# Optimization experiments

Hardware: AMD Instinct MI355X
Metric: run time of the kernel (lower is better)

The kernel has to match this reference:

```python
import jax, jax.numpy as jnp
import numpy as np
import math

N_HEAD = 8
LN_EPS = 1e-5


def _layernorm(x, g, b):
    mu = jnp.mean(x, axis=-1, keepdims=True)
    var = jnp.mean(jnp.square(x - mu), axis=-1, keepdims=True)
    return (x - mu) / jnp.sqrt(var + LN_EPS) * g + b


def setup_inputs() -> dict:
    key0 = jax.random.key(0)
    ks = jax.random.split(key0, 12)
    B, L, D, E = 4, 512, 256, 5  # batch, agents, n_embd, edge_feats_dim

    def w(k, shape):
        return jax.random.normal(k, shape, dtype=jnp.float32) * 0.02

    return {
        "key": jax.random.normal(ks[0], (B, L, D), jnp.float32),
        "value": jax.random.normal(ks[1], (B, L, D), jnp.float32),
        "query": jax.random.normal(ks[2], (B, L, D), jnp.float32),
        "atten_masks": jax.random.randint(ks[3], (B, L, L), 0, 2).astype(jnp.int32),
        "edge_feats": jax.random.normal(ks[4], (B, L, L, E), jnp.float32),
        # Linear weights stored [in, out] so forward is x @ W + b
        "Wk": w(ks[5], (D, D)), "bk": jnp.zeros((D,), jnp.float32),
        "Wq": w(ks[6], (D, D)), "bq": jnp.zeros((D,), jnp.float32),
        "Wv": w(ks[7], (D, D)), "bv": jnp.zeros((D,), jnp.float32),
        "Wp": w(ks[8], (D, D)), "bp": jnp.zeros((D,), jnp.float32),
        "We1": w(ks[9], (E, D)), "be1": jnp.zeros((D,), jnp.float32),
        "ln_g": jnp.ones((D,), jnp.float32), "ln_b": jnp.zeros((D,), jnp.float32),
        "We2": w(ks[10], (D, N_HEAD)), "be2": jnp.zeros((N_HEAD,), jnp.float32),
    }


def reference(key, value, query, atten_masks, edge_feats,
              Wk, bk, Wq, bq, Wv, bv, Wp, bp,
              We1, be1, ln_g, ln_b, We2, be2):
    B, L, D = query.shape
    hd = D // N_HEAD
    # QKV projections -> [B, H, L, hd]
    q = (query @ Wq + bq).reshape(B, L, N_HEAD, hd).transpose(0, 2, 1, 3)
    k = (key @ Wk + bk).reshape(B, L, N_HEAD, hd).transpose(0, 2, 1, 3)
    v = (value @ Wv + bv).reshape(B, L, N_HEAD, hd).transpose(0, 2, 1, 3)
    # scaled attention scores [B, H, L, L]
    att = jnp.einsum('bhqd,bhkd->bhqk', q, k) * (1.0 / math.sqrt(hd))
    # edge-feature additive bias: Linear -> ReLU -> LayerNorm -> Linear(per-head)
    e = jax.nn.relu(edge_feats @ We1 + be1)          # [B, L, L, D]
    e = _layernorm(e, ln_g, ln_b)
    e = e @ We2 + be2                                # [B, L, L, H]
    att = att + e.transpose(0, 3, 1, 2)
    # additive mask (0 -> -inf), softmax over keys
    att = jnp.where(atten_masks[:, None, :, :] == 0, -jnp.inf, att)
    att = jax.nn.softmax(att, axis=-1)
    y = jnp.einsum('bhqk,bhkd->bhqd', att, v)        # [B, H, L, hd]
    y = y.transpose(0, 2, 1, 3).reshape(B, L, D)
    return y @ Wp + bp
```

## Files before the change

### kernel.cpp

```cpp
#include <hip/hip_runtime.h>
#include <hip/hip_bf16.h>

#define L_SEQ 512
#define D_EMB 256
#define NH 8
#define HD 32
#define LL (L_SEQ * L_SEQ)

typedef __attribute__((ext_vector_type(8))) short short8;
typedef __attribute__((ext_vector_type(4))) float f32x4;
typedef unsigned short ushort;

__device__ __forceinline__ float bf2f(ushort u) {
    unsigned int x = ((unsigned int)u) << 16;
    float f;
    __builtin_memcpy(&f, &x, 4);
    return f;
}
__device__ __forceinline__ ushort f2bf(float x) {
    __hip_bfloat16 h = __float2bfloat16(x);
    ushort u;
    __builtin_memcpy(&u, &h, 2);
    return u;
}
__device__ __forceinline__ unsigned int fbits(float x) {
    unsigned int u;
    __builtin_memcpy(&u, &x, 4);
    return u;
}
__device__ __forceinline__ float asf(unsigned int u) {
    float f;
    __builtin_memcpy(&f, &u, 4);
    return f;
}
__device__ __forceinline__ unsigned int pack_bf16rnd(float a, float b) {
    return __builtin_amdgcn_perm(fbits(b) + 0x8000u, fbits(a) + 0x8000u, 0x07060302u);
}
__device__ __forceinline__ uint2 cvt_hilo2(float v0, float v1) {
    unsigned int hi = pack_bf16rnd(v0, v1);
    float h0 = asf(hi << 16);
    float h1 = asf(hi & 0xffff0000u);
    unsigned int lo = pack_bf16rnd(v0 - h0, v1 - h1);
    uint2 r; r.x = hi; r.y = lo;
    return r;
}

__global__ __launch_bounds__(256) void prep_kernel(
    const float* __restrict__ We1, const float* __restrict__ be1,
    const float* __restrict__ g,   const float* __restrict__ bta,
    const float* __restrict__ We2, const float* __restrict__ be2,
    ushort* __restrict__ W1G, ushort* __restrict__ B2G, float* __restrict__ tail)
{
    int t = threadIdx.x;
    __shared__ float red[16][256];
    float gd = g[t], bd = bta[t];
#pragma unroll
    for (int h = 0; h < 8; ++h) {
        float w2 = We2[t * 8 + h];
        red[h][t] = gd * w2;
        red[8 + h][t] = bd * w2;
    }
    __syncthreads();
    for (int off = 128; off > 0; off >>= 1) {
        if (t < off) {
#pragma unroll
            for (int row = 0; row < 16; ++row) red[row][t] += red[row][t + off];
        }
        __syncthreads();
    }
    if (t < 8) {
        tail[t] = red[t][0];
        tail[8 + t] = red[8 + t][0] + be2[t];
    }
    if (t >= 16 && t < 32) tail[t] = 0.f;

    for (int idx = t; idx < 8192; idx += 256) {
        int j = idx & 7, lane = (idx >> 3) & 63, tile = idx >> 9;
        int m = lane & 15, q = lane >> 4;
        int k = q * 8 + j;
        int d = tile * 16 + m;
        float v = 0.f;
        bool lo = false;
        if (k < 5)        v = We1[k * 256 + d];
        else if (k < 10)  { v = We1[(k - 5) * 256 + d]; lo = true; }
        else if (k < 15)  v = We1[(k - 10) * 256 + d];
        else if (k == 15) v = be1[d];
        else if (k == 16) { v = be1[d]; lo = true; }
        ushort hi = f2bf(v);
        W1G[idx] = lo ? f2bf(v - bf2f(hi)) : hi;
    }
    for (int idx = t; idx < 4096; idx += 256) {
        int j = idx & 7, lane = (idx >> 3) & 63, kc = idx >> 9;
        int n = lane & 15, q = lane >> 4;
        int d = kc * 32 + q * 8 + j;
        ushort out;
        if (n < 8)       out = f2bf(g[d] * We2[d * 8 + n]);
        else if (n == 8) out = 0x3F80;
        else             out = 0;
        B2G[idx] = out;
    }
}

__global__ __launch_bounds__(256) void prep_w(
    const float* __restrict__ Wq, const float* __restrict__ Wk,
    const float* __restrict__ Wv, const float* __restrict__ Wp,
    ushort* __restrict__ WThi, ushort* __restrict__ WTlo)
{
    int w = blockIdx.x;
    const float* W = (w == 0) ? Wq : (w == 1) ? Wk : (w == 2) ? Wv : Wp;
    ushort* dh = WThi + (size_t)w * 65536;
    ushort* dl = WTlo + (size_t)w * 65536;

    int tid = threadIdx.x;
    int n = blockIdx.y * 16 + (tid >> 4);
    int k0 = (tid & 15) * 16;

    ushort hbuf[16], lbuf[16];
#pragma unroll
    for (int kk = 0; kk < 16; ++kk) {
        float v = W[(size_t)(k0 + kk) * 256 + n];
        unsigned int hb = fbits(v) + 0x8000u;
        ushort hi = (ushort)(hb >> 16);
        float res = v - bf2f(hi);
        hbuf[kk] = hi;
        lbuf[kk] = (ushort)((fbits(res) + 0x8000u) >> 16);
    }
    *(short8*)(dh + (size_t)n * 256 + k0)     = *(short8*)&hbuf[0];
    *(short8*)(dh + (size_t)n * 256 + k0 + 8) = *(short8*)&hbuf[8];
    *(short8*)(dl + (size_t)n * 256 + k0)     = *(short8*)&lbuf[0];
    *(short8*)(dl + (size_t)n * 256 + k0 + 8) = *(short8*)&lbuf[8];
}

__global__ __launch_bounds__(256) void gemm_mfma(
    const float* __restrict__ A0, const ushort* __restrict__ H0,
    const ushort* __restrict__ L0, const float* __restrict__ b0,
    float* __restrict__ C0,
    const float* __restrict__ A1, const ushort* __restrict__ H1,
    const ushort* __restrict__ L1, const float* __restrict__ b1,
    float* __restrict__ C1,
    const float* __restrict__ A2, const ushort* __restrict__ H2,
    const ushort* __restrict__ L2, const float* __restrict__ b2,
    float* __restrict__ C2)
{
    const float* A; const ushort* BH; const ushort* BL;
    const float* bias; float* C;
    if (blockIdx.z == 0)      { A = A0; BH = H0; BL = L0; bias = b0; C = C0; }
    else if (blockIdx.z == 1) { A = A1; BH = H1; BL = L1; bias = b1; C = C1; }
    else                      { A = A2; BH = H2; BL = L2; bias = b2; C = C2; }

    __shared__ ushort Ahi[64][40];
    __shared__ ushort Alo[64][40];

    int tid = threadIdx.x;
    int wv = tid >> 6, lane = tid & 63;
    int m = lane & 15, quad = lane >> 4;
    int bm = blockIdx.x * 64, bn = blockIdx.y * 64;

    int sm = tid >> 2, sg = (tid & 3) * 8;
    const float* Arow = A + (size_t)(bm + sm) * 256 + sg;

    int nrow = bn + wv * 16 + m;
    const ushort* bhp = BH + (size_t)nrow * 256 + quad * 8;
    const ushort* blp = BL + (size_t)nrow * 256 + quad * 8;

    f32x4 acc[4];
#pragma unroll
    for (int mt = 0; mt < 4; ++mt) acc[mt] = (f32x4){0.f, 0.f, 0.f, 0.f};

    for (int k0 = 0; k0 < 256; k0 += 32) {
        float4 a0 = *(const float4*)(Arow + k0);
        float4 a1 = *(const float4*)(Arow + k0 + 4);
        uint2 c0 = cvt_hilo2(a0.x, a0.y);
        uint2 c1 = cvt_hilo2(a0.z, a0.w);
        uint2 c2 = cvt_hilo2(a1.x, a1.y);
        uint2 c3 = cvt_hilo2(a1.z, a1.w);
        if (k0) __syncthreads();
        uint4 hq; hq.x = c0.x; hq.y = c1.x; hq.z = c2.x; hq.w = c3.x;
        uint4 lq; lq.x = c0.y; lq.y = c1.y; lq.z = c2.y; lq.w = c3.y;
        *(uint4*)&Ahi[sm][sg] = hq;
        *(uint4*)&Alo[sm][sg] = lq;
        __syncthreads();

        short8 bhi = *(const short8*)(bhp + k0);
        short8 blo = *(const short8*)(blp + k0);
#pragma unroll
        for (int mt = 0; mt < 4; ++mt) {
            short8 ahi = *(const short8*)&Ahi[mt * 16 + m][quad * 8];
            short8 alo = *(const short8*)&Alo[mt * 16 + m][quad * 8];
            acc[mt] = __builtin_amdgcn_mfma_f32_16x16x32_bf16(ahi, blo, acc[mt], 0, 0, 0);
            acc[mt] = __builtin_amdgcn_mfma_f32_16x16x32_bf16(alo, bhi, acc[mt], 0, 0, 0);
            acc[mt] = __builtin_amdgcn_mfma_f32_16x16x32_bf16(ahi, bhi, acc[mt], 0, 0, 0);
        }
    }

    float bn_bias = bias[nrow];
#pragma unroll
    for (int mt = 0; mt < 4; ++mt) {
#pragma unroll
        for (int r = 0; r < 4; ++r) {
            C[(size_t)(bm + mt * 16 + quad * 4 + r) * 256 + nrow] = acc[mt][r] + bn_bias;
        }
    }
}

__global__ __launch_bounds__(256) void transpose_k(
    const float* __restrict__ Kw, float* __restrict__ Kt)
{
    __shared__ float tile[128][33];
    int bh = blockIdx.x;
    int b = bh >> 3, h = bh & 7;
    int l0 = blockIdx.y * 128;
    int tid = threadIdx.x;

    int tr = tid >> 3;
    int tc = (tid & 7) * 4;
#pragma unroll
    for (int p = 0; p < 4; ++p) {
        int ll = p * 32 + tr;
        float4 v = *(const float4*)(Kw + ((size_t)(b * L_SEQ + l0 + ll)) * 256 + h * HD + tc);
        tile[ll][tc + 0] = v.x; tile[ll][tc + 1] = v.y;
        tile[ll][tc + 2] = v.z; tile[ll][tc + 3] = v.w;
    }
    __syncthreads();

    float* out = Kt + (size_t)bh * (HD * L_SEQ);
#pragma unroll
    for (int it = 0; it < 16; ++it) {
        int flat = it * 256 + tid;
        int d = flat >> 7;
        int l = flat & 127;
        out[(size_t)d * L_SEQ + l0 + l] = tile[l][d];
    }
}

__global__ __launch_bounds__(256) void edge_bias_mfma(
    const float* __restrict__ EF, const ushort* __restrict__ W1G,
    const ushort* __restrict__ B2G, const float* __restrict__ tail,
    ushort* __restrict__ E2)
{
    __shared__ __align__(16) char xt[4 * 16 * 528];
    int tid = threadIdx.x;
    int wv = tid >> 6, lane = tid & 63;
    int q = lane >> 4, n = lane & 15;
    char* myx = xt + wv * (16 * 528);

    int bi = blockIdx.x;
    int b = bi >> 9, i = bi & 511;
    size_t rowbase = (size_t)bi * 512;

    short8 w1f[16];
#pragma unroll
    for (int t = 0; t < 16; ++t)
        w1f[t] = *(const short8*)(W1G + (t * 64 + lane) * 8);
    short8 b2f[8];
#pragma unroll
    for (int kc = 0; kc < 8; ++kc)
        b2f[kc] = *(const short8*)(B2G + (kc * 64 + lane) * 8);

    float shv = tail[n];
    float bbv = tail[8 + n];
    const ushort ONE = 0x3F80;
    const float inv256 = 1.0f / 256.0f;

    for (int iter = 0; iter < 8; ++iter) {
        int jb = iter * 64 + wv * 16;
        const float* efp = EF + (rowbase + jb + n) * 5;
        float ev[5];
#pragma unroll
        for (int e = 0; e < 5; ++e) ev[e] = efp[e];

        ushort hh[5], llo[5];
#pragma unroll
        for (int e = 0; e < 5; ++e) {
            ushort hi = (ushort)(fbits(ev[e]) >> 16);
            hh[e] = hi;
            llo[e] = (ushort)((fbits(ev[e] - bf2f(hi)) + 0x8000u) >> 16);
        }
        short8 ef8;
        ef8[0] = (short)(q == 0 ? hh[0] : q == 1 ? hh[3] : q == 2 ? ONE : 0);
        ef8[1] = (short)(q == 0 ? hh[1] : q == 1 ? hh[4] : 0);
        ef8[2] = (short)(q == 0 ? hh[2] : q == 1 ? llo[0] : 0);
        ef8[3] = (short)(q == 0 ? hh[3] : q == 1 ? llo[1] : 0);
        ef8[4] = (short)(q == 0 ? hh[4] : q == 1 ? llo[2] : 0);
        ef8[5] = (short)(q == 0 ? hh[0] : q == 1 ? llo[3] : 0);
        ef8[6] = (short)(q == 0 ? hh[1] : q == 1 ? llo[4] : 0);
        ef8[7] = (short)(q == 0 ? hh[2] : q == 1 ? ONE : 0);

#pragma unroll
        for (int t = 0; t < 16; ++t) {
            f32x4 z = {0.f, 0.f, 0.f, 0.f};
            f32x4 d1 = __builtin_amdgcn_mfma_f32_16x16x32_bf16(w1f[t], ef8, z, 0, 0, 0);
            float x0 = fmaxf(d1[0], 0.f);
            float x1 = fmaxf(d1[1], 0.f);
            float x2 = fmaxf(d1[2], 0.f);
            float x3 = fmaxf(d1[3], 0.f);
            uint2 pk;
            pk.x = pack_bf16rnd(x0, x1);
            pk.y = pack_bf16rnd(x2, x3);
            *(uint2*)(myx + n * 528 + t * 32 + q * 8) = pk;
        }

        f32x4 acc  = {0.f, 0.f, 0.f, 0.f};
        f32x4 acc2 = {0.f, 0.f, 0.f, 0.f};
#pragma unroll
        for (int kc = 0; kc < 8; ++kc) {
            short8 a = *(const short8*)(myx + n * 528 + kc * 64 + q * 16);
            acc  = __builtin_amdgcn_mfma_f32_16x16x32_bf16(a, b2f[kc], acc, 0, 0, 0);
            acc2 = __builtin_amdgcn_mfma_f32_16x16x32_bf16(a, a, acc2, 0, 0, 0);
        }

        int base = lane & 48;
        float er[4];
#pragma unroll
        for (int r = 0; r < 4; ++r) {
            float sm = __shfl(acc[r], base + 8);
            float sq = __shfl(acc2[r], base + (base >> 2) + r);
            float dot = acc[r];
            float mu = sm * inv256;
            float var = fmaf(-mu, mu, sq * inv256);
            float rs = rsqrtf(var + 1e-5f);
            er[r] = fmaf(dot - mu * shv, rs, bbv);
        }
        if (n < 8) {
            uint2 outv;
            outv.x = pack_bf16rnd(er[0], er[1]);
            outv.y = pack_bf16rnd(er[2], er[3]);
            size_t basep = (((size_t)(b * NH + n) * L_SEQ + i) * L_SEQ) + jb + q * 4;
            *(uint2*)(E2 + basep) = outv;
        }
    }
}

__global__ __launch_bounds__(256, 3) void attn_kernel(
    const float* __restrict__ Q, const float* __restrict__ Kt,
    const float* __restrict__ V, const ushort* __restrict__ E2,
    const int* __restrict__ MSK, float* __restrict__ Y)
{
    __shared__ float stage[4096];
    __shared__ float pbuf[4][4][520];
    __shared__ float qs_t[32][16];

    int bh = blockIdx.x;
    int b = bh >> 3, h = bh & 7;
    int tid = threadIdx.x;
    int wv = tid >> 6, lane = tid & 63;
    int i0 = blockIdx.y * 16;
    int i = i0 + wv * 4;

    const float* Ktb = Kt + (size_t)bh * (HD * L_SEQ);
    const float* Vb  = V + (size_t)b * L_SEQ * D_EMB + h * HD;

    size_t erow = ((size_t)bh * L_SEQ + i) * L_SEQ;
    size_t mrow = ((size_t)b * L_SEQ + i) * L_SEQ;

    unsigned int e2p[4][4];
    int2 mkp[4][4];
#pragma unroll
    for (int r = 0; r < 4; ++r)
#pragma unroll
        for (int c = 0; c < 4; ++c) {
            int j = c * 128 + 2 * lane;
            e2p[r][c] = *(const unsigned int*)(E2 + erow + (size_t)r * L_SEQ + j);
            mkp[r][c] = *(const int2*)(MSK + mrow + (size_t)r * L_SEQ + j);
        }

    if (tid < 128) {
        int r = tid >> 3, c4 = (tid & 7) * 4;
        float4 qv = *(const float4*)(Q + ((size_t)(b * L_SEQ + i0 + r)) * 256 + h * HD + c4);
        qs_t[c4 + 0][r] = qv.x; qs_t[c4 + 1][r] = qv.y;
        qs_t[c4 + 2][r] = qv.z; qs_t[c4 + 3][r] = qv.w;
    }

    float s[4][8];
#pragma unroll
    for (int r = 0; r < 4; ++r)
#pragma unroll
        for (int t = 0; t < 8; ++t) s[r][t] = 0.f;

    for (int c = 0; c < 4; ++c) {
        if (c) __syncthreads();
        {
            int d0 = tid >> 5, jj = (tid & 31) * 4;
#pragma unroll
            for (int p = 0; p < 4; ++p) {
                int d = p * 8 + d0;
                float4 kv = *(const float4*)(Ktb + (size_t)d * L_SEQ + c * 128 + jj);
                *(float4*)&stage[d * 128 + jj] = kv;
            }
        }
        __syncthreads();
        int c2 = c * 2;
#pragma unroll 8
        for (int d = 0; d < HD; ++d) {
            float4 q4 = *(const float4*)&qs_t[d][wv * 4];
            float2 kv = *(const float2*)&stage[d * 128 + 2 * lane];
            s[0][c2]     = fmaf(q4.x, kv.x, s[0][c2]);
            s[0][c2 + 1] = fmaf(q4.x, kv.y, s[0][c2 + 1]);
            s[1][c2]     = fmaf(q4.y, kv.x, s[1][c2]);
            s[1][c2 + 1] = fmaf(q4.y, kv.y, s[1][c2 + 1]);
            s[2][c2]     = fmaf(q4.z, kv.x, s[2][c2]);
            s[2][c2 + 1] = fmaf(q4.z, kv.y, s[2][c2 + 1]);
            s[3][c2]     = fmaf(q4.w, kv.x, s[3][c2]);
            s[3][c2 + 1] = fmaf(q4.w, kv.y, s[3][c2 + 1]);
        }
    }

    const float scl = 0.17677669529663687f;
#pragma unroll
    for (int r = 0; r < 4; ++r) {
        float sv[8];
        float m = -3.0e38f;
#pragma unroll
        for (int idx = 0; idx < 8; ++idx) {
            int c = idx >> 1, u = idx & 1;
            unsigned int pk = e2p[r][c];
            float e = bf2f((ushort)(u ? (pk >> 16) : (pk & 0xffff)));
            int mk = u ? mkp[r][c].y : mkp[r][c].x;
            float v = (mk != 0) ? fmaf(s[r][idx], scl, e) : -1e30f;
            sv[idx] = v;
            m = fmaxf(m, v);
        }
#pragma unroll
        for (int o = 32; o > 0; o >>= 1) m = fmaxf(m, __shfl_xor(m, o));
        float ssum = 0.f;
#pragma unroll
        for (int idx = 0; idx < 8; ++idx) {
            float p = __expf(sv[idx] - m);
            sv[idx] = p;
            ssum += p;
        }
#pragma unroll
        for (int o = 32; o > 0; o >>= 1) ssum += __shfl_xor(ssum, o);
        float inv = 1.0f / ssum;
#pragma unroll
        for (int c = 0; c < 4; ++c) {
            float2 w;
            w.x = sv[c * 2] * inv;
            w.y = sv[c * 2 + 1] * inv;
            *(float2*)&pbuf[wv][r][c * 128 + 2 * lane] = w;
        }
    }

    int dg = lane >> 3, js = lane & 7;
    float4 acc[4];
#pragma unroll
    for (int r = 0; r < 4; ++r) { acc[r].x = 0.f; acc[r].y = 0.f; acc[r].z = 0.f; acc[r].w = 0.f; }

    for (int c = 0; c < 4; ++c) {
        __syncthreads();
        {
            int j0 = tid >> 3, dd = (tid & 7) * 4;
#pragma unroll
            for (int p = 0; p < 4; ++p) {
                int j = p * 32 + j0;
                float4 vv = *(const float4*)(Vb + (size_t)(c * 128 + j) * D_EMB + dd);
                *(float4*)&stage[j * 32 + dd] = vv;
            }
        }
        __syncthreads();
#pragma unroll
        for (int jb = 0; jb < 16; ++jb) {
            int jj = jb * 8 + js;
            float4 v4 = *(const float4*)&stage[jj * 32 + dg * 4];
#pragma unroll
            for (int r = 0; r < 4; ++r) {
                float p = pbuf[wv][r][c * 128 + jj];
                acc[r].x = fmaf(p, v4.x, acc[r].x);
                acc[r].y = fmaf(p, v4.y, acc[r].y);
                acc[r].z = fmaf(p, v4.z, acc[r].z);
                acc[r].w = fmaf(p, v4.w, acc[r].w);
            }
        }
    }

#pragma unroll
    for (int off = 1; off < 8; off <<= 1) {
#pragma unroll
        for (int r = 0; r < 4; ++r) {
            acc[r].x += __shfl_xor(acc[r].x, off);
            acc[r].y += __shfl_xor(acc[r].y, off);
            acc[r].z += __shfl_xor(acc[r].z, off);
            acc[r].w += __shfl_xor(acc[r].w, off);
        }
    }
    if (js == 0) {
#pragma unroll
        for (int r = 0; r < 4; ++r)
            *(float4*)(Y + ((size_t)(b * L_SEQ + i + r)) * 256 + h * HD + dg * 4) = acc[r];
    }
}

extern "C" void kernel_launch(void* const* d_in, const int* in_sizes, int n_in,
                              void* d_out, int out_size, void* d_ws, size_t ws_size,
                              hipStream_t stream)
{
    const float* key   = (const float*)d_in[0];
    const float* value = (const float*)d_in[1];
    const float* query = (const float*)d_in[2];
    const int*   msk   = (const int*)d_in[3];
    const float* ef    = (const float*)d_in[4];
    const float* Wk  = (const float*)d_in[5];  const float* bk  = (const float*)d_in[6];
    const float* Wq  = (const float*)d_in[7];  const float* bq  = (const float*)d_in[8];
    const float* Wv  = (const float*)d_in[9];  const float* bv  = (const float*)d_in[10];
    const float* Wp  = (const float*)d_in[11]; const float* bp  = (const float*)d_in[12];
    const float* We1 = (const float*)d_in[13]; const float* be1 = (const float*)d_in[14];
    const float* lng = (const float*)d_in[15]; const float* lnb = (const float*)d_in[16];
    const float* We2 = (const float*)d_in[17]; const float* be2 = (const float*)d_in[18];

    const int MTOK = 4 * L_SEQ;
    const int NELT = MTOK * D_EMB;

    float* ws    = (float*)d_ws;
    float* Qw    = ws;
    float* Kw    = Qw + NELT;
    float* Vw    = Kw + NELT;
    float* Yw    = Vw + NELT;
    float* Ktw   = Yw + NELT;
    ushort* W1G  = (ushort*)(Ktw + NELT);
    ushort* B2G  = W1G + 8192;
    float* tail  = (float*)(B2G + 4096);
    ushort* WThi = (ushort*)(tail + 32);
    ushort* WTlo = WThi + 4 * 65536;
    ushort* E2   = WTlo + 4 * 65536;

    hipLaunchKernelGGL(prep_kernel, dim3(1), dim3(256), 0, stream,
                       We1, be1, lng, lnb, We2, be2, W1G, B2G, tail);
    hipLaunchKernelGGL(prep_w, dim3(4, 16), dim3(256), 0, stream,
                       Wq, Wk, Wv, Wp, WThi, WTlo);
    hipLaunchKernelGGL(gemm_mfma, dim3(32, 4, 3), dim3(256), 0, stream,
                       query, WThi + 0 * 65536, WTlo + 0 * 65536, bq, Qw,
                       key,   WThi + 1 * 65536, WTlo + 1 * 65536, bk, Kw,
                       value, WThi + 2 * 65536, WTlo + 2 * 65536, bv, Vw);
    hipLaunchKernelGGL(transpose_k, dim3(32, 4), dim3(256), 0, stream,
                       Kw, Ktw);
    hipLaunchKernelGGL(edge_bias_mfma, dim3(2048), dim3(256), 0, stream,
                       ef, W1G, B2G, tail, E2);
    hipLaunchKernelGGL(attn_kernel, dim3(32, 32), dim3(256), 0, stream,
                       Qw, Ktw, Vw, E2, msk, Yw);
    hipLaunchKernelGGL(gemm_mfma, dim3(32, 4, 1), dim3(256), 0, stream,
                       Yw, WThi + 3 * 65536, WTlo + 3 * 65536, bp, (float*)d_out,
                       Yw, WThi + 3 * 65536, WTlo + 3 * 65536, bp, (float*)d_out,
                       Yw, WThi + 3 * 65536, WTlo + 3 * 65536, bp, (float*)d_out);
}
```

Baseline: 237.6 us.

## Fuse weight prep and K transpose into existing kernels, prefetch edge features

Merges the weight hi/lo splitting into the prep kernel as extra blocks and drops the separate transpose kernel. The K projection GEMM now writes its output directly in transposed layout. Edge-bias kernel prefetches next iteration's edge features, builds bf16 packed operands with perm instructions, and stores LDS in 16-byte chunks. It also permutes the W1G column mapping to match the new LDS layout. This removes two launches and a global round trip of K, at the cost of more complex indexing and strided transposed stores.

```diff
diff --git a/kernel.cpp b/kernel.cpp
--- a/kernel.cpp
+++ b/kernel.cpp
@@ -35,6 +35,9 @@
 }
 __device__ __forceinline__ unsigned int pack_bf16rnd(float a, float b) {
     return __builtin_amdgcn_perm(fbits(b) + 0x8000u, fbits(a) + 0x8000u, 0x07060302u);
+}
+__device__ __forceinline__ unsigned int packhi(unsigned int y, unsigned int x) {
+    return __builtin_amdgcn_perm(y, x, 0x07060302u);
 }
 __device__ __forceinline__ uint2 cvt_hilo2(float v0, float v1) {
     unsigned int hi = pack_bf16rnd(v0, v1);
@@ -49,9 +52,37 @@
     const float* __restrict__ We1, const float* __restrict__ be1,
     const float* __restrict__ g,   const float* __restrict__ bta,
     const float* __restrict__ We2, const float* __restrict__ be2,
-    ushort* __restrict__ W1G, ushort* __restrict__ B2G, float* __restrict__ tail)
+    const float* __restrict__ Wq, const float* __restrict__ Wk,
+    const float* __restrict__ Wv, const float* __restrict__ Wp,
+    ushort* __restrict__ W1G, ushort* __restrict__ B2G, float* __restrict__ tail,
+    ushort* __restrict__ WThi, ushort* __restrict__ WTlo)
 {
     int t = threadIdx.x;
+    if (blockIdx.x != 0) {
+        int bx = blockIdx.x - 1;
+        int w = bx >> 4, ny = bx & 15;
+        const float* W = (w == 0) ? Wq : (w == 1) ? Wk : (w == 2) ? Wv : Wp;
+        ushort* dh = WThi + (size_t)w * 65536;
+        ushort* dl = WTlo + (size_t)w * 65536;
+        int n = ny * 16 + (t >> 4);
+        int k0 = (t & 15) * 16;
+        ushort hbuf[16], lbuf[16];
+#pragma unroll
+        for (int kk = 0; kk < 16; ++kk) {
+            float v = W[(size_t)(k0 + kk) * 256 + n];
+            unsigned int hb = fbits(v) + 0x8000u;
+            ushort hi = (ushort)(hb >> 16);
+            float res = v - bf2f(hi);
+            hbuf[kk] = hi;
+            lbuf[kk] = (ushort)((fbits(res) + 0x8000u) >> 16);
+        }
+        *(short8*)(dh + (size_t)n * 256 + k0)     = *(short8*)&hbuf[0];
+        *(short8*)(dh + (size_t)n * 256 + k0 + 8) = *(short8*)&hbuf[8];
+        *(short8*)(dl + (size_t)n * 256 + k0)     = *(short8*)&lbuf[0];
+        *(short8*)(dl + (size_t)n * 256 + k0 + 8) = *(short8*)&lbuf[8];
+        return;
+    }
+
     __shared__ float red[16][256];
     float gd = g[t], bd = bta[t];
 #pragma unroll
@@ -78,7 +109,7 @@
         int j = idx & 7, lane = (idx >> 3) & 63, tile = idx >> 9;
         int m = lane & 15, q = lane >> 4;
         int k = q * 8 + j;
-        int d = tile * 16 + m;
+        int d = (m >> 2) * 64 + tile * 4 + (m & 3);
         float v = 0.f;
         bool lo = false;
         if (k < 5)        v = We1[k * 256 + d];
@@ -101,52 +132,22 @@
     }
 }
 
-__global__ __launch_bounds__(256) void prep_w(
-    const float* __restrict__ Wq, const float* __restrict__ Wk,
-    const float* __restrict__ Wv, const float* __restrict__ Wp,
-    ushort* __restrict__ WThi, ushort* __restrict__ WTlo)
-{
-    int w = blockIdx.x;
-    const float* W = (w == 0) ? Wq : (w == 1) ? Wk : (w == 2) ? Wv : Wp;
-    ushort* dh = WThi + (size_t)w * 65536;
-    ushort* dl = WTlo + (size_t)w * 65536;
-
-    int tid = threadIdx.x;
-    int n = blockIdx.y * 16 + (tid >> 4);
-    int k0 = (tid & 15) * 16;
-
-    ushort hbuf[16], lbuf[16];
-#pragma unroll
-    for (int kk = 0; kk < 16; ++kk) {
-        float v = W[(size_t)(k0 + kk) * 256 + n];
-        unsigned int hb = fbits(v) + 0x8000u;
-        ushort hi = (ushort)(hb >> 16);
-        float res = v - bf2f(hi);
-        hbuf[kk] = hi;
-        lbuf[kk] = (ushort)((fbits(res) + 0x8000u) >> 16);
-    }
-    *(short8*)(dh + (size_t)n * 256 + k0)     = *(short8*)&hbuf[0];
-    *(short8*)(dh + (size_t)n * 256 + k0 + 8) = *(short8*)&hbuf[8];
-    *(short8*)(dl + (size_t)n * 256 + k0)     = *(short8*)&lbuf[0];
-    *(short8*)(dl + (size_t)n * 256 + k0 + 8) = *(short8*)&lbuf[8];
-}
-
 __global__ __launch_bounds__(256) void gemm_mfma(
     const float* __restrict__ A0, const ushort* __restrict__ H0,
     const ushort* __restrict__ L0, const float* __restrict__ b0,
-    float* __restrict__ C0,
+    float* __restrict__ C0, float* __restrict__ T0,
     const float* __restrict__ A1, const ushort* __restrict__ H1,
     const ushort* __restrict__ L1, const float* __restrict__ b1,
-    float* __restrict__ C1,
+    float* __restrict__ C1, float* __restrict__ T1,
     const float* __restrict__ A2, const ushort* __restrict__ H2,
     const ushort* __restrict__ L2, const float* __restrict__ b2,
-    float* __restrict__ C2)
+    float* __restrict__ C2, float* __restrict__ T2)
 {
     const float* A; const ushort* BH; const ushort* BL;
-    const float* bias; float* C;
-    if (blockIdx.z == 0)      { A = A0; BH = H0; BL = L0; bias = b0; C = C0; }
-    else if (blockIdx.z == 1) { A = A1; BH = H1; BL = L1; bias = b1; C = C1; }
-    else                      { A = A2; BH = H2; BL = L2; bias = b2; C = C2; }
+    const float* bias; float* C; float* Ct;
+    if (blockIdx.z == 0)      { A = A0; BH = H0; BL = L0; bias = b0; C = C0; Ct = T0; }
+    else if (blockIdx.z == 1) { A = A1; BH = H1; BL = L1; bias = b1; C = C1; Ct = T1; }
+    else                      { A = A2; BH = H2; BL = L2; bias = b2; C = C2; Ct = T2; }
 
     __shared__ ushort Ahi[64][40];
     __shared__ ushort Alo[64][40];
@@ -194,42 +195,24 @@
     }
 
     float bn_bias = bias[nrow];
-#pragma unroll
-    for (int mt = 0; mt < 4; ++mt) {
-#pragma unroll
-        for (int r = 0; r < 4; ++r) {
-            C[(size_t)(bm + mt * 16 + quad * 4 + r) * 256 + nrow] = acc[mt][r] + bn_bias;
-        }
-    }
-}
-
-__global__ __launch_bounds__(256) void transpose_k(
-    const float* __restrict__ Kw, float* __restrict__ Kt)
-{
-    __shared__ float tile[128][33];
-    int bh = blockIdx.x;
-    int b = bh >> 3, h = bh & 7;
-    int l0 = blockIdx.y * 128;
-    int tid = threadIdx.x;
-
-    int tr = tid >> 3;
-    int tc = (tid & 7) * 4;
-#pragma unroll
-    for (int p = 0; p < 4; ++p) {
-        int ll = p * 32 + tr;
-        float4 v = *(const float4*)(Kw + ((size_t)(b * L_SEQ + l0 + ll)) * 256 + h * HD + tc);
-        tile[ll][tc + 0] = v.x; tile[ll][tc + 1] = v.y;
-        tile[ll][tc + 2] = v.z; tile[ll][tc + 3] = v.w;
-    }
-    __syncthreads();
-
-    float* out = Kt + (size_t)bh * (HD * L_SEQ);
-#pragma unroll
-    for (int it = 0; it < 16; ++it) {
-        int flat = it * 256 + tid;
-        int d = flat >> 7;
-        int l = flat & 127;
-        out[(size_t)d * L_SEQ + l0 + l] = tile[l][d];
+    if (Ct) {
+        int bb = bm >> 9, l0 = bm & 511;
+        float* outp = Ct + ((size_t)(bb * 256 + nrow)) * 512 + l0 + quad * 4;
+#pragma unroll
+        for (int mt = 0; mt < 4; ++mt) {
+            float4 o;
+            o.x = acc[mt][0] + bn_bias; o.y = acc[mt][1] + bn_bias;
+            o.z = acc[mt][2] + bn_bias; o.w = acc[mt][3] + bn_bias;
+            *(float4*)(outp + mt * 16) = o;
+        }
+    } else {
+#pragma unroll
+        for (int mt = 0; mt < 4; ++mt) {
+#pragma unroll
+            for (int r = 0; r < 4; ++r) {
+                C[(size_t)(bm + mt * 16 + quad * 4 + r) * 256 + nrow] = acc[mt][r] + bn_bias;
+            }
+        }
     }
 }
 
@@ -259,33 +242,56 @@
 
     float shv = tail[n];
     float bbv = tail[8 + n];
-    const ushort ONE = 0x3F80;
     const float inv256 = 1.0f / 256.0f;
 
+    const float* efbase = EF + rowbase * 5;
+    int pairoff = wv * 16 + n;
+
+    float4 evA = *(const float4*)(efbase + (size_t)pairoff * 5);
+    float  evB = efbase[(size_t)pairoff * 5 + 4];
+
     for (int iter = 0; iter < 8; ++iter) {
+        float4 nA; float nB;
+        if (iter < 7) {
+            const float* p = efbase + (size_t)((iter + 1) * 64 + pairoff) * 5;
+            nA = *(const float4*)p;
+            nB = p[4];
+        }
         int jb = iter * 64 + wv * 16;
-        const float* efp = EF + (rowbase + jb + n) * 5;
-        float ev[5];
-#pragma unroll
-        for (int e = 0; e < 5; ++e) ev[e] = efp[e];
-
-        ushort hh[5], llo[5];
-#pragma unroll
-        for (int e = 0; e < 5; ++e) {
-            ushort hi = (ushort)(fbits(ev[e]) >> 16);
-            hh[e] = hi;
-            llo[e] = (ushort)((fbits(ev[e] - bf2f(hi)) + 0x8000u) >> 16);
-        }
+
+        unsigned int hb[5], la[5];
+        hb[0] = fbits(evA.x); hb[1] = fbits(evA.y); hb[2] = fbits(evA.z);
+        hb[3] = fbits(evA.w); hb[4] = fbits(evB);
+        {
+            float e0 = evA.x - asf(hb[0] & 0xffff0000u);
+            float e1 = evA.y - asf(hb[1] & 0xffff0000u);
+            float e2 = evA.z - asf(hb[2] & 0xffff0000u);
+            float e3 = evA.w - asf(hb[3] & 0xffff0000u);
+            float e4 = evB   - asf(hb[4] & 0xffff0000u);
+            la[0] = fbits(e0) + 0x8000u;
+            la[1] = fbits(e1) + 0x8000u;
+            la[2] = fbits(e2) + 0x8000u;
+            la[3] = fbits(e3) + 0x8000u;
+            la[4] = fbits(e4) + 0x8000u;
+        }
+        unsigned int A0v = packhi(hb[1], hb[0]);
+        unsigned int A1v = packhi(hb[3], hb[2]);
+        unsigned int A2v = packhi(hb[0], hb[4]);
+        unsigned int A3v = packhi(hb[2], hb[1]);
+        unsigned int B0v = packhi(hb[4], hb[3]);
+        unsigned int B1v = packhi(la[1], la[0]);
+        unsigned int B2v = packhi(la[3], la[2]);
+        unsigned int B3v = packhi(0x3F800000u, la[4]);
+        uint4 efd;
+        bool isq0 = (q == 0), isq1 = (q == 1), isq2 = (q == 2);
+        efd.x = isq0 ? A0v : isq1 ? B0v : isq2 ? 0x3F80u : 0u;
+        efd.y = isq0 ? A1v : isq1 ? B1v : 0u;
+        efd.z = isq0 ? A2v : isq1 ? B2v : 0u;
+        efd.w = isq0 ? A3v : isq1 ? B3v : 0u;
         short8 ef8;
-        ef8[0] = (short)(q == 0 ? hh[0] : q == 1 ? hh[3] : q == 2 ? ONE : 0);
-        ef8[1] = (short)(q == 0 ? hh[1] : q == 1 ? hh[4] : 0);
-        ef8[2] = (short)(q == 0 ? hh[2] : q == 1 ? llo[0] : 0);
-        ef8[3] = (short)(q == 0 ? hh[3] : q == 1 ? llo[1] : 0);
-        ef8[4] = (short)(q == 0 ? hh[4] : q == 1 ? llo[2] : 0);
-        ef8[5] = (short)(q == 0 ? hh[0] : q == 1 ? llo[3] : 0);
-        ef8[6] = (short)(q == 0 ? hh[1] : q == 1 ? llo[4] : 0);
-        ef8[7] = (short)(q == 0 ? hh[2] : q == 1 ? ONE : 0);
-
+        __builtin_memcpy(&ef8, &efd, 16);
+
+        unsigned int pk0 = 0, pk1 = 0;
 #pragma unroll
         for (int t = 0; t < 16; ++t) {
             f32x4 z = {0.f, 0.f, 0.f, 0.f};
@@ -294,10 +300,14 @@
             float x1 = fmaxf(d1[1], 0.f);
             float x2 = fmaxf(d1[2], 0.f);
             float x3 = fmaxf(d1[3], 0.f);
-            uint2 pk;
-            pk.x = pack_bf16rnd(x0, x1);
-            pk.y = pack_bf16rnd(x2, x3);
-            *(uint2*)(myx + n * 528 + t * 32 + q * 8) = pk;
+            unsigned int pa = pack_bf16rnd(x0, x1);
+            unsigned int pb = pack_bf16rnd(x2, x3);
+            if (t & 1) {
+                uint4 wq; wq.x = pk0; wq.y = pk1; wq.z = pa; wq.w = pb;
+                *(uint4*)(myx + n * 528 + q * 128 + (t - 1) * 8) = wq;
+            } else {
+                pk0 = pa; pk1 = pb;
+            }
         }
 
         f32x4 acc  = {0.f, 0.f, 0.f, 0.f};
@@ -328,6 +338,7 @@
             size_t basep = (((size_t)(b * NH + n) * L_SEQ + i) * L_SEQ) + jb + q * 4;
             *(uint2*)(E2 + basep) = outv;
         }
+        evA = nA; evB = nB;
     }
 }
 
@@ -512,8 +523,7 @@
 
     float* ws    = (float*)d_ws;
     float* Qw    = ws;
-    float* Kw    = Qw + NELT;
-    float* Vw    = Kw + NELT;
+    float* Vw    = Qw + NELT;
     float* Yw    = Vw + NELT;
     float* Ktw   = Yw + NELT;
     ushort* W1G  = (ushort*)(Ktw + NELT);
@@ -523,22 +533,20 @@
     ushort* WTlo = WThi + 4 * 65536;
     ushort* E2   = WTlo + 4 * 65536;
 
-    hipLaunchKernelGGL(prep_kernel, dim3(1), dim3(256), 0, stream,
-                       We1, be1, lng, lnb, We2, be2, W1G, B2G, tail);
-    hipLaunchKernelGGL(prep_w, dim3(4, 16), dim3(256), 0, stream,
-                       Wq, Wk, Wv, Wp, WThi, WTlo);
+    hipLaunchKernelGGL(prep_kernel, dim3(65), dim3(256), 0, stream,
+                       We1, be1, lng, lnb, We2, be2,
+                       Wq, Wk, Wv, Wp,
+                       W1G, B2G, tail, WThi, WTlo);
     hipLaunchKernelGGL(gemm_mfma, dim3(32, 4, 3), dim3(256), 0, stream,
-                       query, WThi + 0 * 65536, WTlo + 0 * 65536, bq, Qw,
-                       key,   WThi + 1 * 65536, WTlo + 1 * 65536, bk, Kw,
-                       value, WThi + 2 * 65536, WTlo + 2 * 65536, bv, Vw);
-    hipLaunchKernelGGL(transpose_k, dim3(32, 4), dim3(256), 0, stream,
-                       Kw, Ktw);
+                       query, WThi + 0 * 65536, WTlo + 0 * 65536, bq, Qw,  (float*)nullptr,
+                       key,   WThi + 1 * 65536, WTlo + 1 * 65536, bk, (float*)nullptr, Ktw,
+                       value, WThi + 2 * 65536, WTlo + 2 * 65536, bv, Vw,  (float*)nullptr);
     hipLaunchKernelGGL(edge_bias_mfma, dim3(2048), dim3(256), 0, stream,
                        ef, W1G, B2G, tail, E2);
     hipLaunchKernelGGL(attn_kernel, dim3(32, 32), dim3(256), 0, stream,
                        Qw, Ktw, Vw, E2, msk, Yw);
     hipLaunchKernelGGL(gemm_mfma, dim3(32, 4, 1), dim3(256), 0, stream,
-                       Yw, WThi + 3 * 65536, WTlo + 3 * 65536, bp, (float*)d_out,
-                       Yw, WThi + 3 * 65536, WTlo + 3 * 65536, bp, (float*)d_out,
-                       Yw, WThi + 3 * 65536, WTlo + 3 * 65536, bp, (float*)d_out);
-}
+                       Yw, WThi + 3 * 65536, WTlo + 3 * 65536, bp, (float*)d_out, (float*)nullptr,
+                       Yw, WThi + 3 * 65536, WTlo + 3 * 65536, bp, (float*)d_out, (float*)nullptr,
+                       Yw, WThi + 3 * 65536, WTlo + 3 * 65536, bp, (float*)d_out, (float*)nullptr);
+}
```

New measurement: 228.5 us. 1.04x faster.
